# Kernel tuning notes

Hardware: AMD Instinct MI355X
Metric: run time of the kernel (lower is better)

## Reference

```python
import jax, jax.numpy as jnp
import numpy as np


def conv3x3(y, w, b):
    # y: [1, Cin, H, W], w: [Cout, Cin, 3, 3] -> [1, Cout, H, W], stride 1, pad 1
    out = jax.lax.conv_general_dilated(
        y, w, window_strides=(1, 1), padding='SAME',
        dimension_numbers=('NCHW', 'OIHW', 'NCHW'))
    return out + b[None, :, None, None]


def setup_inputs() -> dict:
    key = jax.random.key(0)
    ks = jax.random.split(key, 8)
    N, Cin, Cy, H, W, inter = 1024, 1024, 256, 128, 128, 256
    x = jax.random.normal(ks[0], (N, Cin), dtype=jnp.float32)
    y = jax.random.normal(ks[1], (1, Cy, H, W), dtype=jnp.float32)
    # weights initialized ~N(0, 0.01) as in the torch module; biases zero
    g_w = jax.random.normal(ks[2], (inter, Cy, 3, 3), dtype=jnp.float32) * 0.01
    g_b = jnp.zeros((inter,), dtype=jnp.float32)
    phi_w = jax.random.normal(ks[3], (inter, Cy, 3, 3), dtype=jnp.float32) * 0.01
    phi_b = jnp.zeros((inter,), dtype=jnp.float32)
    theta_w = jax.random.normal(ks[4], (inter, Cin), dtype=jnp.float32) * 0.01
    theta_b = jnp.zeros((inter,), dtype=jnp.float32)
    concat_w = jax.random.normal(ks[5], (1, 2 * inter, 1, 1), dtype=jnp.float32) * 0.01
    gamma = jnp.ones((1,), dtype=jnp.float32)  # torch inits 0; use 1 for nontrivial output
    return {"x": x, "y": y, "g_w": g_w, "g_b": g_b, "phi_w": phi_w,
            "phi_b": phi_b, "theta_w": theta_w, "theta_b": theta_b,
            "concat_w": concat_w, "gamma": gamma}


def reference(x, y, g_w, g_b, phi_w, phi_b, theta_w, theta_b, concat_w, gamma):
    inter = g_w.shape[0]
    H, W = y.shape[2], y.shape[3]
    g_y = conv3x3(y, g_w, g_b)          # [1, inter, H, W]
    phi_y = conv3x3(y, phi_w, phi_b)    # [1, inter, H, W]
    theta_x = x @ theta_w.T + theta_b   # [N, inter]
    # 1x1 conv over cat([theta repeated, phi repeated], dim=1) decomposes exactly
    # (linearity of the 1x1 conv, no bias) into two dot products + broadcast add,
    # avoiding the [N, 2*inter, H, W] materialization.
    w = concat_w[0, :, 0, 0]            # [2*inter]
    w_t, w_p = w[:inter], w[inter:]
    s_theta = theta_x @ w_t             # [N]
    s_phi = jnp.einsum('chw,c->hw', phi_y[0], w_p).reshape(-1)  # [H*W]
    f = jax.nn.softmax(s_theta[:, None] + s_phi[None, :], axis=1)  # [N, H*W]
    # g_y.squeeze() -> [inter,H,W]; permute(1,2,0).view(H*W, inter)
    g_flat = jnp.transpose(g_y[0], (1, 2, 0)).reshape(H * W, inter)
    z = gamma * (f @ g_flat)            # [N, inter]
    return z
```

## Files before the change

### kernel.cpp

```cpp
#include <hip/hip_runtime.h>

#define HWDIM 128
#define NPIX  (HWDIM * HWDIM)
#define CY    256
#define INTER 256
#define KTAPS 9
#define WEN   (CY * KTAPS)
#define NW1   32
#define NCS   8
#define CPG   32
#define NPART2 256
#define NRG   4


__device__ __forceinline__ float wave_red_sum(float v) {
    #pragma unroll
    for (int s = 32; s > 0; s >>= 1) v += __shfl_down(v, s, 64);
    return v;
}
__device__ __forceinline__ float wave_red_max(float v) {
    #pragma unroll
    for (int s = 32; s > 0; s >>= 1) v = fmaxf(v, __shfl_down(v, s, 64));
    return v;
}

__global__ void k1_wepart(const float* __restrict__ phi_w,
                          const float* __restrict__ concat_w,
                          float* __restrict__ we_part) {
    int b = blockIdx.x, t = threadIdx.x;
    int cg = b / 9, og = b - cg * 9;
    int o = og * 256 + t;
    const float* pw = phi_w + o;
    float acc = 0.f;
    #pragma unroll
    for (int j = 0; j < 8; ++j) {
        int c = cg * 8 + j;
        acc = fmaf(concat_w[INTER + c], pw[c * WEN], acc);
    }
    we_part[cg * WEN + o] = acc;
}

__global__ void k2a_taps(const float* __restrict__ y,
                         const float* __restrict__ we_part,
                         float* __restrict__ A) {
    __shared__ float swe[CPG * KTAPS];
    int t = threadIdx.x;
    int pg = blockIdx.x & 63;
    int cg = blockIdx.x >> 6;

    for (int i = t; i < CPG * KTAPS; i += 256) {
        float s = 0.f;
        #pragma unroll
        for (int p = 0; p < NW1; ++p)
            s += we_part[p * WEN + cg * CPG * KTAPS + i];
        swe[i] = s;
    }
    __syncthreads();

    int pix = pg * 256 + t;
    float acc[KTAPS];
    #pragma unroll
    for (int k = 0; k < KTAPS; ++k) acc[k] = 0.f;

    const float* yp = y + (size_t)cg * CPG * NPIX + pix;
    #pragma unroll 4
    for (int ch = 0; ch < CPG; ++ch) {
        float yv = yp[ch * NPIX];
        const float* wk = swe + ch * KTAPS;
        #pragma unroll
        for (int k = 0; k < KTAPS; ++k)
            acc[k] = fmaf(wk[k], yv, acc[k]);
    }
    #pragma unroll
    for (int k = 0; k < KTAPS; ++k)
        A[(size_t)(cg * KTAPS + k) * NPIX + pix] = acc[k];
}

__global__ void k2b_sphi(const float* __restrict__ A,
                         float* __restrict__ sphi,
                         float* __restrict__ partials) {
    __shared__ float sred[256];
    int t = threadIdx.x;
    int tg = t >> 6, pl = t & 63;
    int pix = blockIdx.x * 64 + pl;
    int h = pix >> 7, w = pix & 127;

    int idx[KTAPS]; bool val[KTAPS];
    #pragma unroll
    for (int kh = 0; kh < 3; ++kh)
        #pragma unroll
        for (int kw = 0; kw < 3; ++kw) {
            int hh = h + kh - 1, ww = w + kw - 1;
            int k = kh * 3 + kw;
            val[k] = ((unsigned)hh < HWDIM) & ((unsigned)ww < HWDIM);
            idx[k] = hh * HWDIM + ww;
        }

    float acc = 0.f;
    #pragma unroll
    for (int cc = 0; cc < 2; ++cc) {
        const float* Ab = A + (size_t)(tg * 2 + cc) * KTAPS * NPIX;
        #pragma unroll
        for (int k = 0; k < KTAPS; ++k)
            if (val[k]) acc += Ab[(size_t)k * NPIX + idx[k]];
    }
    sred[t] = acc;
    __syncthreads();

    if (t < 64) {
        float v = sred[t] + sred[t + 64] + sred[t + 128] + sred[t + 192];
        sphi[blockIdx.x * 64 + t] = v;
        float m = wave_red_max(v);
        float M = __shfl(m, 0, 64);
        float e = expf(v - M);
        float s = wave_red_sum(e);
        if (t == 0) {
            partials[2 * blockIdx.x]     = M;
            partials[2 * blockIdx.x + 1] = s;
        }
    }
}

__global__ void k4_q(const float* __restrict__ y,
                     const float* __restrict__ sphi,
                     const float* __restrict__ partials,
                     float* __restrict__ q_part) {
    __shared__ float sp[34 * 130];
    __shared__ float s4m[4], s4s[4];
    __shared__ float sq4[4][KTAPS];
    int cy = blockIdx.x & 255;
    int rg = blockIdx.x >> 8;
    int t = threadIdx.x;
    int wid = t >> 6, lane = t & 63;

    float m = partials[2 * t], s = partials[2 * t + 1];
    float wm = wave_red_max(m);
    if (lane == 0) s4m[wid] = wm;
    __syncthreads();
    float M = fmaxf(fmaxf(s4m[0], s4m[1]), fmaxf(s4m[2], s4m[3]));
    float sv = s * expf(m - M);
    float wsum = wave_red_sum(sv);
    if (lane == 0) s4s[wid] = wsum;
    __syncthreads();
    float invS = 1.f / (s4s[0] + s4s[1] + s4s[2] + s4s[3]);

    for (int i = t; i < 34 * 130; i += 256) {
        int r = i / 130, col = i - r * 130;
        int gr = rg * 32 + r - 1, gc = col - 1;
        float v = 0.f;
        if ((unsigned)gr < HWDIM && (unsigned)gc < HWDIM)
            v = expf(sphi[gr * HWDIM + gc] - M) * invS;
        sp[i] = v;
    }
    __syncthreads();

    const float* yc = y + (size_t)cy * NPIX;
    float acc[KTAPS];
    #pragma unroll
    for (int k = 0; k < KTAPS; ++k) acc[k] = 0.f;
    int c = t & 127, vg = t >> 7;

    for (int j = 0; j < 4; ++j) {
        int lr0 = vg * 4 + j * 8;
        float pv[6][3];
        #pragma unroll
        for (int u = 0; u < 6; ++u)
            #pragma unroll
            for (int v = 0; v < 3; ++v)
                pv[u][v] = sp[(lr0 + u) * 130 + c + v];
        #pragma unroll
        for (int dr = 0; dr < 4; ++dr) {
            float yv = yc[(rg * 32 + lr0 + dr) * HWDIM + c];
            #pragma unroll
            for (int kh = 0; kh < 3; ++kh)
                #pragma unroll
                for (int kw = 0; kw < 3; ++kw)
                    acc[kh * 3 + kw] = fmaf(pv[dr + 2 - kh][2 - kw], yv,
                                            acc[kh * 3 + kw]);
        }
    }

    #pragma unroll
    for (int k = 0; k < KTAPS; ++k) {
        float v = wave_red_sum(acc[k]);
        if (lane == 0) sq4[wid][k] = v;
    }
    __syncthreads();
    if (t < KTAPS)
        q_part[rg * WEN + cy * KTAPS + t] =
            sq4[0][t] + sq4[1][t] + sq4[2][t] + sq4[3][t];
}

__global__ void k5_row(const float* __restrict__ g_w,
                       const float* __restrict__ q_part,
                       float* __restrict__ row_part) {
    __shared__ float s4[4];
    int t = threadIdx.x;
    int c = blockIdx.x & 255, half = blockIdx.x >> 8;
    int base = half * (WEN / 2);

    const float* gw = g_w + (size_t)c * WEN;
    float acc = 0.f;
    #pragma unroll
    for (int j = 0; j < 5; ++j) {
        int o = base + j * 256 + t;
        if (o < base + WEN / 2) {
            float qv = q_part[o] + q_part[WEN + o] +
                       q_part[2 * WEN + o] + q_part[3 * WEN + o];
            acc = fmaf(gw[o], qv, acc);
        }
    }
    float v = wave_red_sum(acc);
    int wid = t >> 6, lane = t & 63;
    if (lane == 0) s4[wid] = v;
    __syncthreads();
    if (t == 0)
        row_part[half * 256 + c] = s4[0] + s4[1] + s4[2] + s4[3];
}

__global__ void k6_bcast(const float* __restrict__ row_part,
                         const float* __restrict__ g_b,
                         const float* __restrict__ gamma,
                         float* __restrict__ out, int out_size) {
    __shared__ float sr[256];
    int t = threadIdx.x;
    sr[t] = gamma[0] * (g_b[t] + row_part[t] + row_part[256 + t]);
    __syncthreads();
    int gid = blockIdx.x * 256 + t;
    if (gid < out_size) out[gid] = sr[t];
}

extern "C" void kernel_launch(void* const* d_in, const int* in_sizes, int n_in,
                              void* d_out, int out_size, void* d_ws, size_t ws_size,
                              hipStream_t stream) {
    const float* y        = (const float*)d_in[1];
    const float* g_w      = (const float*)d_in[2];
    const float* g_b      = (const float*)d_in[3];
    const float* phi_w    = (const float*)d_in[4];
    const float* concat_w = (const float*)d_in[8];
    const float* gamma    = (const float*)d_in[9];
    float* out = (float*)d_out;

    float* ws       = (float*)d_ws;
    float* we_part  = ws;
    float* A        = we_part + NW1 * WEN;
    float* sphi     = A + (size_t)NCS * KTAPS * NPIX;
    float* partials = sphi + NPIX;
    float* q_part   = partials + 2 * NPART2;
    float* row_part = q_part + NRG * WEN;
    (void)in_sizes; (void)n_in; (void)ws_size;

    hipLaunchKernelGGL(k1_wepart, dim3(288),      dim3(256), 0, stream,
                       phi_w, concat_w, we_part);
    hipLaunchKernelGGL(k2a_taps,  dim3(64 * NCS), dim3(256), 0, stream,
                       y, we_part, A);
    hipLaunchKernelGGL(k2b_sphi,  dim3(NPART2),   dim3(256), 0, stream,
                       A, sphi, partials);
    hipLaunchKernelGGL(k4_q,      dim3(NRG * CY), dim3(256), 0, stream,
                       y, sphi, partials, q_part);
    hipLaunchKernelGGL(k5_row,    dim3(512),      dim3(256), 0, stream,
                       g_w, q_part, row_part);
    hipLaunchKernelGGL(k6_bcast,  dim3((out_size + 255) / 256), dim3(256), 0,
                       stream, row_part, g_b, gamma, out, out_size);
}
```

Before: 118.5 us.

## Fuse six stage kernels into one cooperative kernel with grid syncs

Replaces the six sequential kernel launches with a single cooperative launch of 512 blocks that separates the stages with grid-wide barriers. This is meant to remove per-launch overhead and inter-kernel gaps. It also changes the q stage so each block handles two y channels, reusing the softmax tile in shared memory, and lets the output broadcast write two rows per thread. The cost is that grid barriers add their own latency, and at least one stage now runs with fewer blocks than before. If the cooperative launch fails, the original multi-kernel path runs instead.

```diff
diff --git a/kernel.cpp b/kernel.cpp
--- a/kernel.cpp
+++ b/kernel.cpp
@@ -1,4 +1,7 @@
 #include <hip/hip_runtime.h>
+#include <hip/hip_cooperative_groups.h>
+
+namespace cg = cooperative_groups;
 
 #define HWDIM 128
 #define NPIX  (HWDIM * HWDIM)
@@ -24,6 +27,226 @@
     return v;
 }
 
+__global__ __launch_bounds__(256, 2)
+void fused_all(const float* __restrict__ y,
+               const float* __restrict__ phi_w,
+               const float* __restrict__ concat_w,
+               const float* __restrict__ g_w,
+               const float* __restrict__ g_b,
+               const float* __restrict__ gamma,
+               float* __restrict__ out, int out_size,
+               float* __restrict__ we_part,
+               float* __restrict__ A,
+               float* __restrict__ sphi,
+               float* __restrict__ partials,
+               float* __restrict__ q_part,
+               float* __restrict__ row_part)
+{
+    cg::grid_group grid = cg::this_grid();
+    __shared__ float smem[4500];
+    const int b = blockIdx.x;
+    const int t = threadIdx.x;
+    const int wid = t >> 6, lane = t & 63;
+
+    if (b < 288) {
+        int cgi = b / 9, og = b - cgi * 9;
+        int o = og * 256 + t;
+        const float* pw = phi_w + o;
+        float acc = 0.f;
+        #pragma unroll
+        for (int j = 0; j < 8; ++j) {
+            int c = cgi * 8 + j;
+            acc = fmaf(concat_w[INTER + c], pw[c * WEN], acc);
+        }
+        we_part[cgi * WEN + o] = acc;
+    }
+    grid.sync();
+
+    {
+        float* swe = smem;
+        const int pg = b & 63, cgi = b >> 6;
+
+        for (int i = t; i < CPG * KTAPS; i += 256) {
+            float s = 0.f;
+            #pragma unroll
+            for (int p = 0; p < NW1; ++p)
+                s += we_part[p * WEN + cgi * CPG * KTAPS + i];
+            swe[i] = s;
+        }
+        __syncthreads();
+
+        int pix = pg * 256 + t;
+        float acc[KTAPS];
+        #pragma unroll
+        for (int k = 0; k < KTAPS; ++k) acc[k] = 0.f;
+
+        const float* yp = y + (size_t)cgi * CPG * NPIX + pix;
+        #pragma unroll 8
+        for (int ch = 0; ch < CPG; ++ch) {
+            float yv = yp[ch * NPIX];
+            const float* wk = swe + ch * KTAPS;
+            #pragma unroll
+            for (int k = 0; k < KTAPS; ++k)
+                acc[k] = fmaf(wk[k], yv, acc[k]);
+        }
+        #pragma unroll
+        for (int k = 0; k < KTAPS; ++k)
+            A[(size_t)(cgi * KTAPS + k) * NPIX + pix] = acc[k];
+    }
+    grid.sync();
+
+    if (b < NPART2) {
+        float* sred = smem;
+        int tg = t >> 6, pl = t & 63;
+        int pix = b * 64 + pl;
+        int h = pix >> 7, w = pix & 127;
+
+        int idx[KTAPS]; bool val[KTAPS];
+        #pragma unroll
+        for (int kh = 0; kh < 3; ++kh)
+            #pragma unroll
+            for (int kw = 0; kw < 3; ++kw) {
+                int hh = h + kh - 1, ww = w + kw - 1;
+                int k = kh * 3 + kw;
+                val[k] = ((unsigned)hh < HWDIM) & ((unsigned)ww < HWDIM);
+                idx[k] = hh * HWDIM + ww;
+            }
+
+        float acc = 0.f;
+        #pragma unroll
+        for (int cc = 0; cc < 2; ++cc) {
+            const float* Ab = A + (size_t)(tg * 2 + cc) * KTAPS * NPIX;
+            #pragma unroll
+            for (int k = 0; k < KTAPS; ++k)
+                if (val[k]) acc += Ab[(size_t)k * NPIX + idx[k]];
+        }
+        sred[t] = acc;
+        __syncthreads();
+
+        if (t < 64) {
+            float v = sred[t] + sred[t + 64] + sred[t + 128] + sred[t + 192];
+            sphi[b * 64 + t] = v;
+            float m = wave_red_max(v);
+            float M = __shfl(m, 0, 64);
+            float e = expf(v - M);
+            float s = wave_red_sum(e);
+            if (t == 0) {
+                partials[2 * b]     = M;
+                partials[2 * b + 1] = s;
+            }
+        }
+    }
+    grid.sync();
+
+    {
+        float* sp  = smem;
+        float* s4m = smem + 4420;
+        float* s4s = smem + 4424;
+        float (*sq4)[18] = (float (*)[18])(smem + 4428);
+        const int rg = b >> 7;
+        const int bc = b & 127;
+        const int cy0 = bc * 2, cy1 = cy0 + 1;
+
+        float m = partials[2 * t], s = partials[2 * t + 1];
+        float wm = wave_red_max(m);
+        if (lane == 0) s4m[wid] = wm;
+        __syncthreads();
+        float M = fmaxf(fmaxf(s4m[0], s4m[1]), fmaxf(s4m[2], s4m[3]));
+        float sv = s * expf(m - M);
+        float wsum = wave_red_sum(sv);
+        if (lane == 0) s4s[wid] = wsum;
+        __syncthreads();
+        float invS = 1.f / (s4s[0] + s4s[1] + s4s[2] + s4s[3]);
+
+        for (int i = t; i < 34 * 130; i += 256) {
+            int r = i / 130, col = i - r * 130;
+            int gr = rg * 32 + r - 1, gc = col - 1;
+            float v = 0.f;
+            if ((unsigned)gr < HWDIM && (unsigned)gc < HWDIM)
+                v = expf(sphi[gr * HWDIM + gc] - M) * invS;
+            sp[i] = v;
+        }
+        __syncthreads();
+
+        const float* yc0 = y + (size_t)cy0 * NPIX;
+        const float* yc1 = y + (size_t)cy1 * NPIX;
+        float acc0[KTAPS], acc1[KTAPS];
+        #pragma unroll
+        for (int k = 0; k < KTAPS; ++k) { acc0[k] = 0.f; acc1[k] = 0.f; }
+        int c = t & 127, vg = t >> 7;
+
+        for (int j = 0; j < 4; ++j) {
+            int lr0 = vg * 4 + j * 8;
+            float pv[6][3];
+            #pragma unroll
+            for (int u = 0; u < 6; ++u)
+                #pragma unroll
+                for (int v = 0; v < 3; ++v)
+                    pv[u][v] = sp[(lr0 + u) * 130 + c + v];
+            #pragma unroll
+            for (int dr = 0; dr < 4; ++dr) {
+                float y0 = yc0[(rg * 32 + lr0 + dr) * HWDIM + c];
+                float y1 = yc1[(rg * 32 + lr0 + dr) * HWDIM + c];
+                #pragma unroll
+                for (int kh = 0; kh < 3; ++kh)
+                    #pragma unroll
+                    for (int kw = 0; kw < 3; ++kw) {
+                        float p = pv[dr + 2 - kh][2 - kw];
+                        acc0[kh * 3 + kw] = fmaf(p, y0, acc0[kh * 3 + kw]);
+                        acc1[kh * 3 + kw] = fmaf(p, y1, acc1[kh * 3 + kw]);
+                    }
+            }
+        }
+
+        #pragma unroll
+        for (int k = 0; k < KTAPS; ++k) {
+            float v0 = wave_red_sum(acc0[k]);
+            float v1 = wave_red_sum(acc1[k]);
+            if (lane == 0) { sq4[wid][k] = v0; sq4[wid][9 + k] = v1; }
+        }
+        __syncthreads();
+        if (t < KTAPS) {
+            q_part[rg * WEN + cy0 * KTAPS + t] =
+                sq4[0][t] + sq4[1][t] + sq4[2][t] + sq4[3][t];
+            q_part[rg * WEN + cy1 * KTAPS + t] =
+                sq4[0][9 + t] + sq4[1][9 + t] + sq4[2][9 + t] + sq4[3][9 + t];
+        }
+    }
+    grid.sync();
+
+    {
+        float* s4 = smem;
+        int c = b & 255, half = b >> 8;
+        int base = half * (WEN / 2);
+
+        const float* gw = g_w + (size_t)c * WEN;
+        float acc = 0.f;
+        #pragma unroll
+        for (int j = 0; j < 5; ++j) {
+            int o = base + j * 256 + t;
+            if (o < base + WEN / 2) {
+                float qv = q_part[o] + q_part[WEN + o] +
+                           q_part[2 * WEN + o] + q_part[3 * WEN + o];
+                acc = fmaf(gw[o], qv, acc);
+            }
+        }
+        float v = wave_red_sum(acc);
+        if (lane == 0) s4[wid] = v;
+        __syncthreads();
+        if (t == 0)
+            row_part[half * 256 + c] = s4[0] + s4[1] + s4[2] + s4[3];
+    }
+    grid.sync();
+
+    {
+        float val = gamma[0] * (g_b[t] + row_part[t] + row_part[256 + t]);
+        int gid0 = b * 256 + t;
+        if (gid0 < out_size) out[gid0] = val;
+        int gid1 = (b + 512) * 256 + t;
+        if (gid1 < out_size) out[gid1] = val;
+    }
+}
+
 __global__ void k1_wepart(const float* __restrict__ phi_w,
                           const float* __restrict__ concat_w,
                           float* __restrict__ we_part) {
@@ -250,16 +473,29 @@
     float* row_part = q_part + NRG * WEN;
     (void)in_sizes; (void)n_in; (void)ws_size;
 
-    hipLaunchKernelGGL(k1_wepart, dim3(288),      dim3(256), 0, stream,
-                       phi_w, concat_w, we_part);
-    hipLaunchKernelGGL(k2a_taps,  dim3(64 * NCS), dim3(256), 0, stream,
-                       y, we_part, A);
-    hipLaunchKernelGGL(k2b_sphi,  dim3(NPART2),   dim3(256), 0, stream,
-                       A, sphi, partials);
-    hipLaunchKernelGGL(k4_q,      dim3(NRG * CY), dim3(256), 0, stream,
-                       y, sphi, partials, q_part);
-    hipLaunchKernelGGL(k5_row,    dim3(512),      dim3(256), 0, stream,
-                       g_w, q_part, row_part);
-    hipLaunchKernelGGL(k6_bcast,  dim3((out_size + 255) / 256), dim3(256), 0,
-                       stream, row_part, g_b, gamma, out, out_size);
-}
+    int osz = out_size;
+    void* args[] = {
+        (void*)&y, (void*)&phi_w, (void*)&concat_w, (void*)&g_w,
+        (void*)&g_b, (void*)&gamma, (void*)&out, (void*)&osz,
+        (void*)&we_part, (void*)&A, (void*)&sphi, (void*)&partials,
+        (void*)&q_part, (void*)&row_part
+    };
+    hipError_t err = hipLaunchCooperativeKernel(
+        reinterpret_cast<void*>(fused_all), dim3(512), dim3(256),
+        args, 0, stream);
+
+    if (err != hipSuccess) {
+        hipLaunchKernelGGL(k1_wepart, dim3(288),      dim3(256), 0, stream,
+                           phi_w, concat_w, we_part);
+        hipLaunchKernelGGL(k2a_taps,  dim3(64 * NCS), dim3(256), 0, stream,
+                           y, we_part, A);
+        hipLaunchKernelGGL(k2b_sphi,  dim3(NPART2),   dim3(256), 0, stream,
+                           A, sphi, partials);
+        hipLaunchKernelGGL(k4_q,      dim3(NRG * CY), dim3(256), 0, stream,
+                           y, sphi, partials, q_part);
+        hipLaunchKernelGGL(k5_row,    dim3(512),      dim3(256), 0, stream,
+                           g_w, q_part, row_part);
+        hipLaunchKernelGGL(k6_bcast,  dim3((out_size + 255) / 256), dim3(256),
+                           0, stream, row_part, g_b, gamma, out, out_size);
+    }
+}
```

Measured after the change: 363.9 us. 3.07x slower.

## Fuse weight-projection into tap kernel, merge row-reduce with broadcast, two channels per block

Applied to the files above, without the earlier changes.

Folds the concat_w·phi_w projection into the tap kernel, so each block recomputes its 288 effective weights directly from phi_w instead of reading a precomputed partial buffer. Merges the g_w row reduction with the output broadcast, cutting the launch count from six to four. The q kernel now handles two y channels per block, halving the number of shared softmax-tile builds, and the tap loop unroll goes from 4 to 8. In exchange, the phi_w reduction is repeated by all 64 pixel-group blocks of each channel group. The output write now strides by 256 floats per thread in kD, which is uncoalesced, and kD uses only 256 blocks.

```diff
diff --git a/kernel.cpp b/kernel.cpp
--- a/kernel.cpp
+++ b/kernel.cpp
@@ -24,35 +24,28 @@
     return v;
 }
 
-__global__ void k1_wepart(const float* __restrict__ phi_w,
-                          const float* __restrict__ concat_w,
-                          float* __restrict__ we_part) {
-    int b = blockIdx.x, t = threadIdx.x;
-    int cg = b / 9, og = b - cg * 9;
-    int o = og * 256 + t;
-    const float* pw = phi_w + o;
-    float acc = 0.f;
-    #pragma unroll
-    for (int j = 0; j < 8; ++j) {
-        int c = cg * 8 + j;
-        acc = fmaf(concat_w[INTER + c], pw[c * WEN], acc);
-    }
-    we_part[cg * WEN + o] = acc;
-}
-
-__global__ void k2a_taps(const float* __restrict__ y,
-                         const float* __restrict__ we_part,
-                         float* __restrict__ A) {
+__global__ void kA_taps(const float* __restrict__ y,
+                        const float* __restrict__ phi_w,
+                        const float* __restrict__ concat_w,
+                        float* __restrict__ A) {
     __shared__ float swe[CPG * KTAPS];
     int t = threadIdx.x;
     int pg = blockIdx.x & 63;
     int cg = blockIdx.x >> 6;
+    const int cgbase = cg * CPG * KTAPS;
 
     for (int i = t; i < CPG * KTAPS; i += 256) {
+        const float* pw = phi_w + cgbase + i;
         float s = 0.f;
-        #pragma unroll
-        for (int p = 0; p < NW1; ++p)
-            s += we_part[p * WEN + cg * CPG * KTAPS + i];
+        for (int p = 0; p < NW1; ++p) {
+            float partial = 0.f;
+            #pragma unroll
+            for (int j = 0; j < 8; ++j) {
+                int c = p * 8 + j;
+                partial = fmaf(concat_w[INTER + c], pw[c * WEN], partial);
+            }
+            s += partial;
+        }
         swe[i] = s;
     }
     __syncthreads();
@@ -63,7 +56,7 @@
     for (int k = 0; k < KTAPS; ++k) acc[k] = 0.f;
 
     const float* yp = y + (size_t)cg * CPG * NPIX + pix;
-    #pragma unroll 4
+    #pragma unroll 8
     for (int ch = 0; ch < CPG; ++ch) {
         float yv = yp[ch * NPIX];
         const float* wk = swe + ch * KTAPS;
@@ -76,9 +69,9 @@
         A[(size_t)(cg * KTAPS + k) * NPIX + pix] = acc[k];
 }
 
-__global__ void k2b_sphi(const float* __restrict__ A,
-                         float* __restrict__ sphi,
-                         float* __restrict__ partials) {
+__global__ void kB_sphi(const float* __restrict__ A,
+                        float* __restrict__ sphi,
+                        float* __restrict__ partials) {
     __shared__ float sred[256];
     int t = threadIdx.x;
     int tg = t >> 6, pl = t & 63;
@@ -121,15 +114,16 @@
     }
 }
 
-__global__ void k4_q(const float* __restrict__ y,
+__global__ void kC_q(const float* __restrict__ y,
                      const float* __restrict__ sphi,
                      const float* __restrict__ partials,
                      float* __restrict__ q_part) {
     __shared__ float sp[34 * 130];
     __shared__ float s4m[4], s4s[4];
-    __shared__ float sq4[4][KTAPS];
-    int cy = blockIdx.x & 255;
-    int rg = blockIdx.x >> 8;
+    __shared__ float sq4[4][2 * KTAPS];
+    const int rg = blockIdx.x >> 7;
+    const int bc = blockIdx.x & 127;
+    const int cy0 = bc * 2, cy1 = cy0 + 1;
     int t = threadIdx.x;
     int wid = t >> 6, lane = t & 63;
 
@@ -154,10 +148,11 @@
     }
     __syncthreads();
 
-    const float* yc = y + (size_t)cy * NPIX;
-    float acc[KTAPS];
-    #pragma unroll
-    for (int k = 0; k < KTAPS; ++k) acc[k] = 0.f;
+    const float* yc0 = y + (size_t)cy0 * NPIX;
+    const float* yc1 = y + (size_t)cy1 * NPIX;
+    float acc0[KTAPS], acc1[KTAPS];
+    #pragma unroll
+    for (int k = 0; k < KTAPS; ++k) { acc0[k] = 0.f; acc1[k] = 0.f; }
     int c = t & 127, vg = t >> 7;
 
     for (int j = 0; j < 4; ++j) {
@@ -170,64 +165,79 @@
                 pv[u][v] = sp[(lr0 + u) * 130 + c + v];
         #pragma unroll
         for (int dr = 0; dr < 4; ++dr) {
-            float yv = yc[(rg * 32 + lr0 + dr) * HWDIM + c];
+            float y0 = yc0[(rg * 32 + lr0 + dr) * HWDIM + c];
+            float y1 = yc1[(rg * 32 + lr0 + dr) * HWDIM + c];
             #pragma unroll
             for (int kh = 0; kh < 3; ++kh)
                 #pragma unroll
-                for (int kw = 0; kw < 3; ++kw)
-                    acc[kh * 3 + kw] = fmaf(pv[dr + 2 - kh][2 - kw], yv,
-                                            acc[kh * 3 + kw]);
+                for (int kw = 0; kw < 3; ++kw) {
+                    float p = pv[dr + 2 - kh][2 - kw];
+                    acc0[kh * 3 + kw] = fmaf(p, y0, acc0[kh * 3 + kw]);
+                    acc1[kh * 3 + kw] = fmaf(p, y1, acc1[kh * 3 + kw]);
+                }
         }
     }
 
     #pragma unroll
     for (int k = 0; k < KTAPS; ++k) {
-        float v = wave_red_sum(acc[k]);
-        if (lane == 0) sq4[wid][k] = v;
-    }
-    __syncthreads();
-    if (t < KTAPS)
-        q_part[rg * WEN + cy * KTAPS + t] =
+        float v0 = wave_red_sum(acc0[k]);
+        float v1 = wave_red_sum(acc1[k]);
+        if (lane == 0) { sq4[wid][k] = v0; sq4[wid][KTAPS + k] = v1; }
+    }
+    __syncthreads();
+    if (t < KTAPS) {
+        q_part[rg * WEN + cy0 * KTAPS + t] =
             sq4[0][t] + sq4[1][t] + sq4[2][t] + sq4[3][t];
-}
-
-__global__ void k5_row(const float* __restrict__ g_w,
-                       const float* __restrict__ q_part,
-                       float* __restrict__ row_part) {
-    __shared__ float s4[4];
-    int t = threadIdx.x;
-    int c = blockIdx.x & 255, half = blockIdx.x >> 8;
-    int base = half * (WEN / 2);
+        q_part[rg * WEN + cy1 * KTAPS + t] =
+            sq4[0][KTAPS + t] + sq4[1][KTAPS + t] +
+            sq4[2][KTAPS + t] + sq4[3][KTAPS + t];
+    }
+}
+
+__global__ void kD_zout(const float* __restrict__ g_w,
+                        const float* __restrict__ q_part,
+                        const float* __restrict__ g_b,
+                        const float* __restrict__ gamma,
+                        float* __restrict__ out, int out_size) {
+    __shared__ float s4a[4], s4b[4];
+    int t = threadIdx.x;
+    int c = blockIdx.x;
+    int wid = t >> 6, lane = t & 63;
 
     const float* gw = g_w + (size_t)c * WEN;
-    float acc = 0.f;
+
+    float acc0 = 0.f;
     #pragma unroll
     for (int j = 0; j < 5; ++j) {
-        int o = base + j * 256 + t;
-        if (o < base + WEN / 2) {
+        int o = j * 256 + t;
+        if (o < WEN / 2) {
             float qv = q_part[o] + q_part[WEN + o] +
                        q_part[2 * WEN + o] + q_part[3 * WEN + o];
-            acc = fmaf(gw[o], qv, acc);
-        }
-    }
-    float v = wave_red_sum(acc);
-    int wid = t >> 6, lane = t & 63;
-    if (lane == 0) s4[wid] = v;
-    __syncthreads();
-    if (t == 0)
-        row_part[half * 256 + c] = s4[0] + s4[1] + s4[2] + s4[3];
-}
-
-__global__ void k6_bcast(const float* __restrict__ row_part,
-                         const float* __restrict__ g_b,
-                         const float* __restrict__ gamma,
-                         float* __restrict__ out, int out_size) {
-    __shared__ float sr[256];
-    int t = threadIdx.x;
-    sr[t] = gamma[0] * (g_b[t] + row_part[t] + row_part[256 + t]);
-    __syncthreads();
-    int gid = blockIdx.x * 256 + t;
-    if (gid < out_size) out[gid] = sr[t];
+            acc0 = fmaf(gw[o], qv, acc0);
+        }
+    }
+    float acc1 = 0.f;
+    #pragma unroll
+    for (int j = 0; j < 5; ++j) {
+        int o = (WEN / 2) + j * 256 + t;
+        if (o < WEN) {
+            float qv = q_part[o] + q_part[WEN + o] +
+                       q_part[2 * WEN + o] + q_part[3 * WEN + o];
+            acc1 = fmaf(gw[o], qv, acc1);
+        }
+    }
+    float v0 = wave_red_sum(acc0);
+    float v1 = wave_red_sum(acc1);
+    if (lane == 0) { s4a[wid] = v0; s4b[wid] = v1; }
+    __syncthreads();
+    float r0 = s4a[0] + s4a[1] + s4a[2] + s4a[3];
+    float r1 = s4b[0] + s4b[1] + s4b[2] + s4b[3];
+    float val = gamma[0] * (g_b[c] + r0 + r1);
+
+    for (int i = t; i < 1024; i += 256) {
+        int gid = i * 256 + c;
+        if (gid < out_size) out[gid] = val;
+    }
 }
 
 extern "C" void kernel_launch(void* const* d_in, const int* in_sizes, int n_in,
@@ -242,24 +252,18 @@
     float* out = (float*)d_out;
 
     float* ws       = (float*)d_ws;
-    float* we_part  = ws;
-    float* A        = we_part + NW1 * WEN;
+    float* A        = ws;
     float* sphi     = A + (size_t)NCS * KTAPS * NPIX;
     float* partials = sphi + NPIX;
     float* q_part   = partials + 2 * NPART2;
-    float* row_part = q_part + NRG * WEN;
     (void)in_sizes; (void)n_in; (void)ws_size;
 
-    hipLaunchKernelGGL(k1_wepart, dim3(288),      dim3(256), 0, stream,
-                       phi_w, concat_w, we_part);
-    hipLaunchKernelGGL(k2a_taps,  dim3(64 * NCS), dim3(256), 0, stream,
-                       y, we_part, A);
-    hipLaunchKernelGGL(k2b_sphi,  dim3(NPART2),   dim3(256), 0, stream,
+    hipLaunchKernelGGL(kA_taps, dim3(64 * NCS), dim3(256), 0, stream,
+                       y, phi_w, concat_w, A);
+    hipLaunchKernelGGL(kB_sphi, dim3(NPART2),   dim3(256), 0, stream,
                        A, sphi, partials);
-    hipLaunchKernelGGL(k4_q,      dim3(NRG * CY), dim3(256), 0, stream,
+    hipLaunchKernelGGL(kC_q,    dim3(NRG * 128), dim3(256), 0, stream,
                        y, sphi, partials, q_part);
-    hipLaunchKernelGGL(k5_row,    dim3(512),      dim3(256), 0, stream,
-                       g_w, q_part, row_part);
-    hipLaunchKernelGGL(k6_bcast,  dim3((out_size + 255) / 256), dim3(256), 0,
-                       stream, row_part, g_b, gamma, out, out_size);
-}
+    hipLaunchKernelGGL(kD_zout, dim3(CY),       dim3(256), 0, stream,
+                       g_w, q_part, g_b, gamma, out, out_size);
+}
```

Measured after the change: 233.9 us. 1.97x slower.
